# Optimization experiments

Measured on AMD Instinct MI355X. Metric: run time of the kernel, lower is better.

Reference implementation:

```python
import jax, jax.numpy as jnp
import numpy as np

NUM_HEADS = 16
ROPE_THETA = 10000.0


def setup_inputs() -> dict:
    key = jax.random.key(0)
    k1, k2, k3 = jax.random.split(key, 3)
    B, T, C = 2, 2048, 1024
    x = jax.random.normal(k1, (B, T, C), dtype=jnp.float32)
    w_qkv = jax.random.normal(k2, (3 * C, C), dtype=jnp.float32) * 0.02
    w_out = jax.random.normal(k3, (C, C), dtype=jnp.float32) * 0.02
    return {"x": x, "w_qkv": w_qkv, "w_out": w_out}


def _apply_rope(x, cos, sin):
    # x: (B, H, T, D); interleaved complex pairs: (x[...,2i], x[...,2i+1])
    B, H, T, D = x.shape
    xp = x.reshape(B, H, T, D // 2, 2)
    xr, xi = xp[..., 0], xp[..., 1]
    # cos/sin: (T, D//2) broadcast over (B, H)
    out_r = xr * cos - xi * sin
    out_i = xr * sin + xi * cos
    return jnp.stack([out_r, out_i], axis=-1).reshape(B, H, T, D)


def reference(x, w_qkv, w_out):
    B, T, C = x.shape
    H = NUM_HEADS
    D = C // H
    scale = 1.0 / np.sqrt(D).astype(np.float32)

    qkv = x @ w_qkv.T                      # (B, T, 3C)
    q, k, v = jnp.split(qkv, 3, axis=-1)

    def to_heads(t):
        return t.reshape(B, T, H, D).transpose(0, 2, 1, 3)  # (B, H, T, D)

    q, k, v = to_heads(q), to_heads(k), to_heads(v)

    # RoPE frequencies: freqs[t, j] = t / theta^(2j/D)
    inv_freq = 1.0 / (ROPE_THETA ** (jnp.arange(0, D, 2, dtype=jnp.float32) / D))
    freqs = jnp.arange(T, dtype=jnp.float32)[:, None] * inv_freq[None, :]  # (T, D//2)
    cos, sin = jnp.cos(freqs), jnp.sin(freqs)

    q = _apply_rope(q, cos, sin)
    k = _apply_rope(k, cos, sin)

    att = jnp.einsum('bhqd,bhkd->bhqk', q, k) * scale   # (B, H, T, T)
    causal = jnp.tril(jnp.ones((T, T), dtype=bool))
    att = jnp.where(causal[None, None], att, -jnp.inf)
    att = jax.nn.softmax(att, axis=-1)
    # dropout p=0.0 (eval) -> identity

    out = jnp.einsum('bhqk,bhkd->bhqd', att, v)          # (B, H, T, D)
    out = out.transpose(0, 2, 1, 3).reshape(B, T, C)
    return out @ w_out.T
```

## Files before the change

kernel.cpp:

```cpp
#include <hip/hip_runtime.h>
#include <hip/hip_bf16.h>
#include <math.h>

#define DEV __device__ __forceinline__

typedef float  floatx4 __attribute__((ext_vector_type(4)));
typedef short  bf16x8  __attribute__((ext_vector_type(8)));
typedef short  bf16x4  __attribute__((ext_vector_type(4)));

typedef __attribute__((address_space(1))) void gvoid;
typedef __attribute__((address_space(3))) void lvoid;

static constexpr int Bc = 2, Tc = 2048, Cc = 1024, Hc = 16, Dc = 64;

DEV void gload16(const void* g, void* l) {
    __builtin_amdgcn_global_load_lds((gvoid*)g, (lvoid*)l, 16, 0, 0);
}

__global__ void prep_kernel(const float* __restrict__ xf,
                            const float* __restrict__ wqkvf,
                            const float* __restrict__ woutf,
                            __hip_bfloat16* __restrict__ xb,
                            __hip_bfloat16* __restrict__ wqkvb,
                            __hip_bfloat16* __restrict__ woutb,
                            float* __restrict__ cosT, float* __restrict__ sinT) {
    int gb = blockIdx.x;
    if (gb < 8192) {
        const float* src; __hip_bfloat16* dst; int i;
        if (gb < 4096)      { src = xf;    dst = xb;    i = gb * 256 + threadIdx.x; }
        else if (gb < 7168) { src = wqkvf; dst = wqkvb; i = (gb - 4096) * 256 + threadIdx.x; }
        else                { src = woutf; dst = woutb; i = (gb - 7168) * 256 + threadIdx.x; }
        float4 f = ((const float4*)src)[i];
        union { ushort4 u; __hip_bfloat16 h[4]; } pk;
        pk.h[0] = __float2bfloat16(f.x);
        pk.h[1] = __float2bfloat16(f.y);
        pk.h[2] = __float2bfloat16(f.z);
        pk.h[3] = __float2bfloat16(f.w);
        ((ushort4*)dst)[i] = pk.u;
    } else {
        int i = (gb - 8192) * 256 + threadIdx.x;
        int j = i >> 11, t = i & 2047;
        float invf = exp2f((float)j * -0.4152410118609203f);
        float f = (float)t * invf;
        cosT[i] = cosf(f);
        sinT[i] = sinf(f);
    }
}

__global__ __launch_bounds__(256, 2) void gemm_qkv(
    const __hip_bfloat16* __restrict__ A,
    const __hip_bfloat16* __restrict__ Bm,
    __hip_bfloat16* __restrict__ qb,
    __hip_bfloat16* __restrict__ kb,
    __hip_bfloat16* __restrict__ vb,
    const float* __restrict__ cosT,
    const float* __restrict__ sinT,
    int K)
{
    __shared__ __align__(16) __hip_bfloat16 SM[2 * 128 * 64];
    __hip_bfloat16* const As = SM;
    __hip_bfloat16* const Bs = SM + 128 * 64;

    const int tid  = threadIdx.x;
    const int lane = tid & 63, wave = tid >> 6;
    const int quad = lane >> 4, cidx = lane & 15;
    const int wm = wave & 1, wn = wave >> 1;
    const int bm = blockIdx.x * 128, bn = blockIdx.y * 128;

    floatx4 acc[4][4] = {};

    for (int k0 = 0; k0 < K; k0 += 64) {
#pragma unroll
        for (int it = 0; it < 4; ++it) {
            int idx = tid + it * 256;
            int r = idx >> 3, cs = idx & 7;
            int cg = cs ^ (r & 7);
            gload16(A  + (size_t)(bm + r) * K + k0 + cg * 8, As + idx * 8);
            gload16(Bm + (size_t)(bn + r) * K + k0 + cg * 8, Bs + idx * 8);
        }
        __syncthreads();
#pragma unroll
        for (int ks = 0; ks < 2; ++ks) {
            bf16x8 af[4], bf[4];
#pragma unroll
            for (int mt = 0; mt < 4; ++mt) {
                int r = wm * 64 + mt * 16 + cidx;
                af[mt] = *(const bf16x8*)(As + (r * 8 + ((ks * 4 + quad) ^ (r & 7))) * 8);
            }
#pragma unroll
            for (int nt = 0; nt < 4; ++nt) {
                int r = wn * 64 + nt * 16 + cidx;
                bf[nt] = *(const bf16x8*)(Bs + (r * 8 + ((ks * 4 + quad) ^ (r & 7))) * 8);
            }
#pragma unroll
            for (int mt = 0; mt < 4; ++mt)
#pragma unroll
                for (int nt = 0; nt < 4; ++nt)
                    acc[mt][nt] = __builtin_amdgcn_mfma_f32_16x16x32_bf16(
                        af[mt], bf[nt], acc[mt][nt], 0, 0, 0);
        }
        __syncthreads();
    }

    if (bn >= 2048) {
#pragma unroll
        for (int nt = 0; nt < 4; ++nt) {
            int n_l = wn * 64 + nt * 16 + cidx;
#pragma unroll
            for (int mt = 0; mt < 4; ++mt)
#pragma unroll
                for (int reg = 0; reg < 4; ++reg) {
                    int m_l = wm * 64 + mt * 16 + quad * 4 + reg;
                    SM[n_l * 128 + (((m_l >> 3) ^ (n_l & 15)) * 8) + (m_l & 7)] =
                        __float2bfloat16(acc[mt][nt][reg]);
                }
        }
        __syncthreads();
        {
            int b = bm >> 11, t0 = bm & 2047;
            int c = tid & 15;
#pragma unroll
            for (int it = 0; it < 8; ++it) {
                int row = it * 16 + (tid >> 4);
                int cc = (bn - 2048) + row;
                int h = cc >> 6, d = cc & 63;
                *(uint4*)(vb + ((size_t)(b * Hc + h) * Dc + d) * Tc + t0 + c * 8) =
                    *(const uint4*)(SM + row * 128 + ((c ^ (row & 15)) * 8));
            }
        }
    } else {
        const float SL2E = 0.125f * 1.44269504088896f;
        const bool isq = (bn < 1024);
#pragma unroll
        for (int nt = 0; nt < 4; ++nt) {
            int n_l = wn * 64 + nt * 16 + cidx;
            int d = n_l & 63, j = d >> 1;
            const float* cp = cosT + j * 2048;
            const float* sp = sinT + j * 2048;
#pragma unroll
            for (int mt = 0; mt < 4; ++mt) {
                int m0 = wm * 64 + mt * 16 + quad * 4;
                int t0 = (bm + m0) & 2047;
                float4 c4 = *(const float4*)(cp + t0);
                float4 s4 = *(const float4*)(sp + t0);
#pragma unroll
                for (int reg = 0; reg < 4; ++reg) {
                    float v = acc[mt][nt][reg];
                    float p = __shfl_xor(v, 1);
                    float cz = ((const float*)&c4)[reg];
                    float sz = ((const float*)&s4)[reg];
                    float o = (d & 1) ? (p * sz + v * cz) : (v * cz - p * sz);
                    if (isq) o *= SL2E;
                    int m_l = m0 + reg;
                    SM[m_l * 128 + (((n_l >> 3) ^ (m_l & 15)) * 8) + (n_l & 7)] =
                        __float2bfloat16(o);
                }
            }
        }
        __syncthreads();
        {
            __hip_bfloat16* dst = isq ? qb : kb;
            const int bnl = bn & 1023;
#pragma unroll
            for (int it = 0; it < 8; ++it) {
                int c = it * 256 + tid;
                int row = c >> 4, s = c & 15;
                int m = bm + row;
                int b = m >> 11, t = m & 2047;
                int h = (bnl >> 6) + (s >> 3);
                int d0 = (s & 7) * 8;
                *(uint4*)(dst + ((size_t)(b * Hc + h) * Tc + t) * Dc + d0) =
                    *(const uint4*)(SM + row * 128 + ((s ^ (row & 15)) * 8));
            }
        }
    }
}

__global__ __launch_bounds__(256, 2) void gemm_out(
    const __hip_bfloat16* __restrict__ A,
    const __hip_bfloat16* __restrict__ Bm,
    float* __restrict__ Cout)
{
    __shared__ __align__(16) __hip_bfloat16 As[64 * 64];
    __shared__ __align__(16) __hip_bfloat16 Bs[128 * 64];

    const int tid  = threadIdx.x;
    const int lane = tid & 63, wave = tid >> 6;
    const int quad = lane >> 4, cidx = lane & 15;
    const int bm = blockIdx.x * 64, bn = blockIdx.y * 128;
    const int K = 1024;

    floatx4 acc[4][2] = {};

    for (int k0 = 0; k0 < K; k0 += 64) {
        int h = k0 >> 6;
#pragma unroll
        for (int it = 0; it < 2; ++it) {
            int idx = tid + it * 256;
            int r = idx >> 3, cs = idx & 7;
            int cg = cs ^ (r & 7);
            int m = bm + r;
            const __hip_bfloat16* src =
                A + ((size_t)((m >> 11) * 16 + h) * 2048 + (m & 2047)) * 64 + cg * 8;
            gload16(src, As + idx * 8);
        }
#pragma unroll
        for (int it = 0; it < 4; ++it) {
            int idx = tid + it * 256;
            int r = idx >> 3, cs = idx & 7;
            int cg = cs ^ (r & 7);
            gload16(Bm + (size_t)(bn + r) * K + k0 + cg * 8, Bs + idx * 8);
        }
        __syncthreads();
#pragma unroll
        for (int ks = 0; ks < 2; ++ks) {
            bf16x8 af[4], bf[2];
#pragma unroll
            for (int mt = 0; mt < 4; ++mt) {
                int r = mt * 16 + cidx;
                af[mt] = *(const bf16x8*)(As + (r * 8 + ((ks * 4 + quad) ^ (r & 7))) * 8);
            }
#pragma unroll
            for (int nt = 0; nt < 2; ++nt) {
                int r = wave * 32 + nt * 16 + cidx;
                bf[nt] = *(const bf16x8*)(Bs + (r * 8 + ((ks * 4 + quad) ^ (r & 7))) * 8);
            }
#pragma unroll
            for (int mt = 0; mt < 4; ++mt)
#pragma unroll
                for (int nt = 0; nt < 2; ++nt)
                    acc[mt][nt] = __builtin_amdgcn_mfma_f32_16x16x32_bf16(
                        af[mt], bf[nt], acc[mt][nt], 0, 0, 0);
        }
        __syncthreads();
    }

#pragma unroll
    for (int mt = 0; mt < 4; ++mt)
#pragma unroll
        for (int nt = 0; nt < 2; ++nt) {
            int n = bn + wave * 32 + nt * 16 + cidx;
#pragma unroll
            for (int reg = 0; reg < 4; ++reg) {
                int m = bm + mt * 16 + quad * 4 + reg;
                Cout[(size_t)m * 1024 + n] = acc[mt][nt][reg];
            }
        }
}

__global__ __launch_bounds__(256, 2) void attn_kernel(
    const __hip_bfloat16* __restrict__ qb,
    const __hip_bfloat16* __restrict__ kb,
    const __hip_bfloat16* __restrict__ vb,
    __hip_bfloat16* __restrict__ ob)
{
    __shared__ __align__(16) __hip_bfloat16 KB[2 * 128 * 64];
    __shared__ __align__(16) __hip_bfloat16 VB[2 * 64 * 128];

    const int tid  = threadIdx.x;
    const int lane = tid & 63, wave = tid >> 6;
    const int quad = lane >> 4, cidx = lane & 15;
    const int id = blockIdx.x;
    const int xcd = id & 7, s = id >> 3;
    const int bh  = xcd * 4 + (s & 3);
    const int m   = s >> 2;
    const int qt  = (m < 8) ? (15 - m) : (m - 8);
    const int qbase = qt * 128;
    const int ktmax = qt;
    const size_t plane = (size_t)bh * Tc * Dc;
    const __hip_bfloat16* Vp = vb + plane;
    const __hip_bfloat16* Kp = kb + plane;

    __hip_bfloat16* const Qs = KB + 128 * 64;
    __hip_bfloat16* const Os = KB;

#pragma unroll
    for (int it = 0; it < 4; ++it) {
        int idx = tid + it * 256;
        int r = idx >> 3, cg = (idx & 7) ^ (r & 7);
        gload16(qb + plane + (size_t)(qbase + r) * 64 + cg * 8, Qs + idx * 8);
    }
#pragma unroll
    for (int it = 0; it < 4; ++it) {
        int idx = tid + it * 256;
        int r = idx >> 3, cg = (idx & 7) ^ (r & 7);
        gload16(Kp + (size_t)r * 64 + cg * 8, KB + idx * 8);
    }
#pragma unroll
    for (int it = 0; it < 4; ++it) {
        int idx = tid + it * 256;
        int r = idx >> 4, c = (idx & 15) ^ (r & 15);
        gload16(Vp + (size_t)r * Tc + c * 8, VB + idx * 8);
    }
    __syncthreads();

    bf16x8 qf[2][2];
#pragma unroll
    for (int qb2 = 0; qb2 < 2; ++qb2)
#pragma unroll
        for (int ks = 0; ks < 2; ++ks) {
            int r = wave * 32 + qb2 * 16 + cidx;
            qf[qb2][ks] = *(const bf16x8*)(Qs + (r * 8 + ((ks * 4 + quad) ^ (r & 7))) * 8);
        }
    __syncthreads();

    floatx4 oaccT[2][4] = {};
    floatx4 lpart[2] = {};
    const int q0 = qbase + wave * 32 + cidx;

    for (int kt = 0; kt <= ktmax; ++kt) {
        const __hip_bfloat16* Kc = KB + (kt & 1) * (128 * 64);
        const __hip_bfloat16* Vc = VB + (kt & 1) * (64 * 128);

        if (kt < ktmax) {
            __hip_bfloat16* Kn = KB + ((kt + 1) & 1) * (128 * 64);
            __hip_bfloat16* Vn = VB + ((kt + 1) & 1) * (64 * 128);
#pragma unroll
            for (int it = 0; it < 4; ++it) {
                int idx = tid + it * 256;
                int r = idx >> 3, cg = (idx & 7) ^ (r & 7);
                gload16(Kp + (size_t)((kt + 1) * 128 + r) * 64 + cg * 8, Kn + idx * 8);
            }
#pragma unroll
            for (int it = 0; it < 4; ++it) {
                int idx = tid + it * 256;
                int r = idx >> 4, c = (idx & 15) ^ (r & 15);
                gload16(Vp + (size_t)r * Tc + (kt + 1) * 128 + c * 8, Vn + idx * 8);
            }
        }

        floatx4 sacc[2][8] = {};
#pragma unroll
        for (int ks = 0; ks < 2; ++ks)
#pragma unroll
            for (int kb8 = 0; kb8 < 8; ++kb8) {
                int r = kb8 * 16 + cidx;
                bf16x8 af = *(const bf16x8*)(
                    Kc + (r * 8 + ((ks * 4 + quad) ^ (r & 7))) * 8);
                sacc[0][kb8] = __builtin_amdgcn_mfma_f32_16x16x32_bf16(
                    af, qf[0][ks], sacc[0][kb8], 0, 0, 0);
                sacc[1][kb8] = __builtin_amdgcn_mfma_f32_16x16x32_bf16(
                    af, qf[1][ks], sacc[1][kb8], 0, 0, 0);
            }

        const bool domask = (kt == ktmax);
        bf16x4 pf[2][8];
#pragma unroll
        for (int qb2 = 0; qb2 < 2; ++qb2) {
            const int q = q0 + qb2 * 16;
#pragma unroll
            for (int kb8 = 0; kb8 < 8; ++kb8)
#pragma unroll
                for (int reg = 0; reg < 4; ++reg) {
                    int key = kt * 128 + kb8 * 16 + quad * 4 + reg;
                    float p = __builtin_amdgcn_exp2f(sacc[qb2][kb8][reg]);
                    if (domask && key > q) p = 0.0f;
                    lpart[qb2][reg] += p;
                    __hip_bfloat16 hb = __float2bfloat16(p);
                    pf[qb2][kb8][reg] = *(const short*)&hb;
                }
        }

#pragma unroll
        for (int dt = 0; dt < 4; ++dt) {
            int d = dt * 16 + cidx;
#pragma unroll
            for (int c8 = 0; c8 < 8; ++c8) {
                int ch = c8 * 2 + (quad >> 1);
                bf16x4 vtf = *(const bf16x4*)(
                    Vc + (d * 16 + (ch ^ (d & 15))) * 8 + (quad & 1) * 4);
                oaccT[0][dt] = __builtin_amdgcn_mfma_f32_16x16x16bf16_1k(
                    vtf, pf[0][c8], oaccT[0][dt], 0, 0, 0);
                oaccT[1][dt] = __builtin_amdgcn_mfma_f32_16x16x16bf16_1k(
                    vtf, pf[1][c8], oaccT[1][dt], 0, 0, 0);
            }
        }

        __syncthreads();
    }

#pragma unroll
    for (int qb2 = 0; qb2 < 2; ++qb2) {
        float l = lpart[qb2][0] + lpart[qb2][1] + lpart[qb2][2] + lpart[qb2][3];
        l += __shfl_xor(l, 16);
        l += __shfl_xor(l, 32);
        float inv = 1.0f / l;
        int qq = wave * 32 + qb2 * 16 + cidx;
#pragma unroll
        for (int dt = 0; dt < 4; ++dt) {
            bf16x4 o4;
#pragma unroll
            for (int reg = 0; reg < 4; ++reg) {
                __hip_bfloat16 hb = __float2bfloat16(oaccT[qb2][dt][reg] * inv);
                o4[reg] = *(const short*)&hb;
            }
            int g = dt * 4 + quad;
            *(bf16x4*)(Os + qq * 64 + ((g ^ (qq & 12)) * 4)) = o4;
        }
    }
    __syncthreads();
#pragma unroll
    for (int i = 0; i < 4; ++i) {
        int c = tid + i * 256;
        int row = c >> 3, cp = c & 7;
        *(uint4*)(ob + plane + (size_t)(qbase + row) * 64 + cp * 8) =
            *(const uint4*)(Os + row * 64 + ((cp * 2) ^ (row & 12)) * 4);
    }
}

extern "C" void kernel_launch(void* const* d_in, const int* in_sizes, int n_in,
                              void* d_out, int out_size, void* d_ws, size_t ws_size,
                              hipStream_t stream) {
    const float* xf = nullptr; const float* wqkvf = nullptr; const float* woutf = nullptr;
    for (int i = 0; i < n_in; ++i) {
        if      (in_sizes[i] == 2 * 2048 * 1024) xf    = (const float*)d_in[i];
        else if (in_sizes[i] == 3 * 1024 * 1024) wqkvf = (const float*)d_in[i];
        else if (in_sizes[i] == 1024 * 1024)     woutf = (const float*)d_in[i];
    }
    float* out = (float*)d_out;

    char* ws = (char*)d_ws;
    const size_t MB = 1024 * 1024;
    __hip_bfloat16* qb    = (__hip_bfloat16*)(ws);
    __hip_bfloat16* kb    = (__hip_bfloat16*)(ws + 8  * MB);
    __hip_bfloat16* vb    = (__hip_bfloat16*)(ws + 16 * MB);
    __hip_bfloat16* ab    = (__hip_bfloat16*)(ws + 24 * MB);
    float* cosT           = (float*)(ws + 32 * MB);
    float* sinT           = (float*)(ws + 32 * MB + 256 * 1024);
    __hip_bfloat16* xb    = (__hip_bfloat16*)(ws + 33 * MB);
    __hip_bfloat16* wqkvb = (__hip_bfloat16*)(ws + 41 * MB);
    __hip_bfloat16* woutb = (__hip_bfloat16*)(ws + 47 * MB);

    prep_kernel<<<dim3(8448), dim3(256), 0, stream>>>(
        xf, wqkvf, woutf, xb, wqkvb, woutb, cosT, sinT);

    gemm_qkv<<<dim3(32, 24), dim3(256), 0, stream>>>(
        xb, wqkvb, qb, kb, vb, cosT, sinT, 1024);
    attn_kernel<<<dim3(512), dim3(256), 0, stream>>>(qb, kb, vb, ab);
    gemm_out<<<dim3(64, 8), dim3(256), 0, stream>>>(ab, woutb, out);
}
```

Baseline: 164.9 us.

## Read K and V directly from global memory in attention, dropping LDS staging

The attention kernel stops staging K and V tiles in double-buffered shared memory and instead loads MFMA operands straight from global memory (relying on caches), keeping only a small LDS buffer for Q/O. This removes the per-iteration barriers and LDS traffic, and raises the launch-bounds occupancy hint from 2 to 3 blocks per CU. The cost is that each of the four waves in a block now fetches the same K/V data separately through the cache with narrower, less coalesced accesses, and there is no explicit prefetch overlapping loads with compute.

```diff
diff --git a/kernel.cpp b/kernel.cpp
--- a/kernel.cpp
+++ b/kernel.cpp
@@ -248,14 +248,13 @@
         }
 }
 
-__global__ __launch_bounds__(256, 2) void attn_kernel(
+__global__ __launch_bounds__(256, 3) void attn_kernel(
     const __hip_bfloat16* __restrict__ qb,
     const __hip_bfloat16* __restrict__ kb,
     const __hip_bfloat16* __restrict__ vb,
     __hip_bfloat16* __restrict__ ob)
 {
-    __shared__ __align__(16) __hip_bfloat16 KB[2 * 128 * 64];
-    __shared__ __align__(16) __hip_bfloat16 VB[2 * 64 * 128];
+    __shared__ __align__(16) __hip_bfloat16 Os[128 * 64];
 
     const int tid  = threadIdx.x;
     const int lane = tid & 63, wave = tid >> 6;
@@ -271,26 +270,11 @@
     const __hip_bfloat16* Vp = vb + plane;
     const __hip_bfloat16* Kp = kb + plane;
 
-    __hip_bfloat16* const Qs = KB + 128 * 64;
-    __hip_bfloat16* const Os = KB;
-
 #pragma unroll
     for (int it = 0; it < 4; ++it) {
         int idx = tid + it * 256;
         int r = idx >> 3, cg = (idx & 7) ^ (r & 7);
-        gload16(qb + plane + (size_t)(qbase + r) * 64 + cg * 8, Qs + idx * 8);
-    }
-#pragma unroll
-    for (int it = 0; it < 4; ++it) {
-        int idx = tid + it * 256;
-        int r = idx >> 3, cg = (idx & 7) ^ (r & 7);
-        gload16(Kp + (size_t)r * 64 + cg * 8, KB + idx * 8);
-    }
-#pragma unroll
-    for (int it = 0; it < 4; ++it) {
-        int idx = tid + it * 256;
-        int r = idx >> 4, c = (idx & 15) ^ (r & 15);
-        gload16(Vp + (size_t)r * Tc + c * 8, VB + idx * 8);
+        gload16(qb + plane + (size_t)(qbase + r) * 64 + cg * 8, Os + idx * 8);
     }
     __syncthreads();
 
@@ -300,43 +284,22 @@
 #pragma unroll
         for (int ks = 0; ks < 2; ++ks) {
             int r = wave * 32 + qb2 * 16 + cidx;
-            qf[qb2][ks] = *(const bf16x8*)(Qs + (r * 8 + ((ks * 4 + quad) ^ (r & 7))) * 8);
-        }
-    __syncthreads();
+            qf[qb2][ks] = *(const bf16x8*)(Os + (r * 8 + ((ks * 4 + quad) ^ (r & 7))) * 8);
+        }
 
     floatx4 oaccT[2][4] = {};
     floatx4 lpart[2] = {};
     const int q0 = qbase + wave * 32 + cidx;
 
     for (int kt = 0; kt <= ktmax; ++kt) {
-        const __hip_bfloat16* Kc = KB + (kt & 1) * (128 * 64);
-        const __hip_bfloat16* Vc = VB + (kt & 1) * (64 * 128);
-
-        if (kt < ktmax) {
-            __hip_bfloat16* Kn = KB + ((kt + 1) & 1) * (128 * 64);
-            __hip_bfloat16* Vn = VB + ((kt + 1) & 1) * (64 * 128);
-#pragma unroll
-            for (int it = 0; it < 4; ++it) {
-                int idx = tid + it * 256;
-                int r = idx >> 3, cg = (idx & 7) ^ (r & 7);
-                gload16(Kp + (size_t)((kt + 1) * 128 + r) * 64 + cg * 8, Kn + idx * 8);
-            }
-#pragma unroll
-            for (int it = 0; it < 4; ++it) {
-                int idx = tid + it * 256;
-                int r = idx >> 4, c = (idx & 15) ^ (r & 15);
-                gload16(Vp + (size_t)r * Tc + (kt + 1) * 128 + c * 8, Vn + idx * 8);
-            }
-        }
-
         floatx4 sacc[2][8] = {};
 #pragma unroll
         for (int ks = 0; ks < 2; ++ks)
 #pragma unroll
             for (int kb8 = 0; kb8 < 8; ++kb8) {
-                int r = kb8 * 16 + cidx;
                 bf16x8 af = *(const bf16x8*)(
-                    Kc + (r * 8 + ((ks * 4 + quad) ^ (r & 7))) * 8);
+                    Kp + (size_t)(kt * 128 + kb8 * 16 + cidx) * 64
+                       + (ks * 4 + quad) * 8);
                 sacc[0][kb8] = __builtin_amdgcn_mfma_f32_16x16x32_bf16(
                     af, qf[0][ks], sacc[0][kb8], 0, 0, 0);
                 sacc[1][kb8] = __builtin_amdgcn_mfma_f32_16x16x32_bf16(
@@ -363,20 +326,17 @@
 
 #pragma unroll
         for (int dt = 0; dt < 4; ++dt) {
-            int d = dt * 16 + cidx;
+            const __hip_bfloat16* vrow =
+                Vp + (size_t)(dt * 16 + cidx) * Tc + kt * 128 + quad * 4;
 #pragma unroll
             for (int c8 = 0; c8 < 8; ++c8) {
-                int ch = c8 * 2 + (quad >> 1);
-                bf16x4 vtf = *(const bf16x4*)(
-                    Vc + (d * 16 + (ch ^ (d & 15))) * 8 + (quad & 1) * 4);
+                bf16x4 vtf = *(const bf16x4*)(vrow + c8 * 16);
                 oaccT[0][dt] = __builtin_amdgcn_mfma_f32_16x16x16bf16_1k(
                     vtf, pf[0][c8], oaccT[0][dt], 0, 0, 0);
                 oaccT[1][dt] = __builtin_amdgcn_mfma_f32_16x16x16bf16_1k(
                     vtf, pf[1][c8], oaccT[1][dt], 0, 0, 0);
             }
         }
-
-        __syncthreads();
     }
 
 #pragma unroll
```

Measured after the change: 232.6 us. +41.0%, slower.
